# Performance work log

Measured on AMD Instinct MI355X. Metric: run time of the kernel, lower is better.

## Reference

```python
import jax, jax.numpy as jnp
import numpy as np

N_LUT_IN = 4  # fan-in of every LUT node (the 'n' init arg)
KSIZE = 3


def _lut_level(x, w):
    """x: [O, N, L*n] in [0,1]; w: [O, L, 2^n] LUT tables -> [O, N, L].
    Differentiable LUT = multilinear interpolation over the 2^n corners."""
    O, L = w.shape[0], w.shape[1]
    xi = x.reshape(x.shape[0], x.shape[1], L, N_LUT_IN)
    # iterative doubling builds corner probs without a [.., 2^n, n] broadcast
    p = jnp.ones(xi.shape[:3] + (1,), xi.dtype)
    for i in range(N_LUT_IN):
        xii = xi[..., i:i + 1]
        p = jnp.concatenate([p * (1.0 - xii), p * xii], axis=-1)  # [O,N,L,2^i+1]
    return jnp.einsum('onlc,olc->onl', p, w)


def _lut_tree(flat, ws):
    """flat: [O, N, n_leaf_inputs]; ws: list of per-level LUT tables [O, L_lvl, 16]."""
    x = jax.nn.sigmoid(flat)  # squash real activations into [0,1] for interpolation
    for li, w in enumerate(ws):
        need = w.shape[1] * N_LUT_IN
        pad = need - x.shape[-1]
        if pad > 0:  # pad with 0.5 == sigmoid(0), matching zero-padding of raw inputs
            x = jnp.pad(x, ((0, 0), (0, 0), (0, pad)), constant_values=0.5)
        x = _lut_level(x, w)
        if li < len(ws) - 1:
            x = jax.nn.sigmoid(x)
    return x[..., 0]  # [O, N]


def setup_inputs() -> dict:
    key = jax.random.key(0)
    ks = jax.random.split(key, 5)
    B, C, H, W = 8, 64, 32, 32
    O, Q = 32, 8
    x = jax.random.normal(ks[0], (B, C, H, W), jnp.float32)
    rng = np.random.default_rng(0)
    ci = jnp.asarray(np.stack([rng.permutation(C)[:Q] for _ in range(O)]), jnp.int32)
    # tree level widths for 72 leaf inputs, fan-in 4: 72 -> 18 -> 5 -> 2 -> 1
    w0 = jax.random.normal(ks[1], (O, 18, 16), jnp.float32) * 0.5
    w1 = jax.random.normal(ks[2], (O, 5, 16), jnp.float32) * 0.5
    w2 = jax.random.normal(ks[3], (O, 2, 16), jnp.float32) * 0.5
    w3 = jax.random.normal(ks[4], (O, 1, 16), jnp.float32) * 0.5
    return {'x': x, 'w0': w0, 'w1': w1, 'w2': w2, 'w3': w3, 'channel_indices': ci}


def reference(x, w0, w1, w2, w3, channel_indices):
    B, C, H, W = x.shape
    K = KSIZE
    # unfold: pad=1, stride=1 -> [B, C*K*K, Ho, Wo], feature dim is channel-major (C, K, K)
    patches = jax.lax.conv_general_dilated_patches(
        x, (K, K), (1, 1), ((1, 1), (1, 1)))
    Ho, Wo = patches.shape[2], patches.shape[3]
    patches = patches.reshape(B, C, K, K, Ho, Wo)
    O, Q = channel_indices.shape
    sel = patches[:, channel_indices]  # per-out-channel gather: [B, O, Q, K, K, Ho, Wo]
    # match torch permute(0,2,3,1,4,5): leaf order per pixel is (channel, kh, kw)
    flat = sel.transpose(1, 0, 5, 6, 2, 3, 4).reshape(O, B * Ho * Wo, Q * K * K)
    out = _lut_tree(flat, [w0, w1, w2, w3])  # [O, B*Ho*Wo]
    return out.reshape(O, B, Ho, Wo).transpose(1, 0, 2, 3)  # [B, O, Ho, Wo]
```

## Files before the change

### kernel.cpp

```cpp
#include <hip/hip_runtime.h>

#define O_DIM 32
#define Q_DIM 8
#define HW 32

__device__ __forceinline__ float sigmoidf(float v) {
    return __builtin_amdgcn_rcpf(1.0f + __expf(-v));
}

__device__ __forceinline__ float lut4(float s0, float s1, float s2, float s3,
                                      const float* __restrict__ W) {
    float a[8];
#pragma unroll
    for (int j = 0; j < 8; ++j) a[j] = fmaf(s3, W[j + 8] - W[j], W[j]);
#pragma unroll
    for (int j = 0; j < 4; ++j) a[j] = fmaf(s2, a[j + 4] - a[j], a[j]);
#pragma unroll
    for (int j = 0; j < 2; ++j) a[j] = fmaf(s1, a[j + 2] - a[j], a[j]);
    return fmaf(s0, a[1] - a[0], a[0]);
}

__global__ __launch_bounds__(256) void lt_conv_kernel(
    const float* __restrict__ x,
    const float* __restrict__ w0,
    const float* __restrict__ w1,
    const float* __restrict__ w2,
    const float* __restrict__ w3,
    const int*   __restrict__ ci,
    float*       __restrict__ out)
{
    const int bid  = blockIdx.x;
    const int tile = bid & 3;
    const int b    = (bid >> 2) & 7;
    const int o    = bid >> 5;

    const int tid = threadIdx.x;
    const int wo  = tid & 31;
    const int ho  = tile * 8 + (tid >> 5);

    float s[72];
#pragma unroll
    for (int q = 0; q < Q_DIM; ++q) {
        const int c = ci[o * Q_DIM + q];
        const float* xc = x + (size_t)(b * 64 + c) * (HW * HW);
#pragma unroll
        for (int dy = 0; dy < 3; ++dy) {
            const int y = ho + dy - 1;
            const bool yok = (unsigned)y < (unsigned)HW;
#pragma unroll
            for (int dx = 0; dx < 3; ++dx) {
                const int xx = wo + dx - 1;
                const bool ok = yok && ((unsigned)xx < (unsigned)HW);
                const float v = ok ? xc[y * HW + xx] : 0.0f;
                s[q * 9 + dy * 3 + dx] = sigmoidf(v);
            }
        }
    }

    const float* W0 = w0 + o * 18 * 16;
    float t[18];
#pragma unroll
    for (int l = 0; l < 18; ++l)
        t[l] = sigmoidf(lut4(s[4*l], s[4*l+1], s[4*l+2], s[4*l+3], W0 + l*16));

    const float* W1 = w1 + o * 5 * 16;
    float u[5];
#pragma unroll
    for (int l = 0; l < 4; ++l)
        u[l] = sigmoidf(lut4(t[4*l], t[4*l+1], t[4*l+2], t[4*l+3], W1 + l*16));
    u[4] = sigmoidf(lut4(t[16], t[17], 0.5f, 0.5f, W1 + 4*16));

    const float* W2 = w2 + o * 2 * 16;
    const float v0 = sigmoidf(lut4(u[0], u[1], u[2], u[3], W2));
    const float v1 = sigmoidf(lut4(u[4], 0.5f, 0.5f, 0.5f, W2 + 16));

    const float* W3 = w3 + o * 16;
    const float r = lut4(v0, v1, 0.5f, 0.5f, W3);

    out[((size_t)(b * O_DIM + o) * HW + ho) * HW + wo] = r;
}

extern "C" void kernel_launch(void* const* d_in, const int* in_sizes, int n_in,
                              void* d_out, int out_size, void* d_ws, size_t ws_size,
                              hipStream_t stream) {
    const float* x  = (const float*)d_in[0];
    const float* w0 = (const float*)d_in[1];
    const float* w1 = (const float*)d_in[2];
    const float* w2 = (const float*)d_in[3];
    const float* w3 = (const float*)d_in[4];
    const int*   ci = (const int*)d_in[5];
    float* out = (float*)d_out;

    dim3 grid(O_DIM * 8 * 4);
    dim3 block(256);
    lt_conv_kernel<<<grid, block, 0, stream>>>(x, w0, w1, w2, w3, ci, out);
}
```

Before: 83.68 us.

## Stage sigmoid-ed padded input tile in LDS and compute two rows per thread with packed FMA

Each block now covers a full 32x32 image for one (o,b) pair. It loads the 8 selected channels with a one-pixel halo into shared memory and applies the sigmoid once per input element, instead of once per 3x3 window tap. Each thread evaluates the LUT tree for two vertically adjacent pixels using 2-wide float vectors, which lets the compiler emit packed FMAs. The goal is to remove the 9x redundant global loads and sigmoids. The trade-offs are fewer blocks (256), about 37KB of LDS per block, and higher register pressure.

```diff
diff --git a/kernel.cpp b/kernel.cpp
--- a/kernel.cpp
+++ b/kernel.cpp
@@ -1,26 +1,34 @@
 #include <hip/hip_runtime.h>
 
-#define O_DIM 32
-#define Q_DIM 8
+typedef float v2f __attribute__((ext_vector_type(2)));
+
 #define HW 32
+#define QD 8
 
 __device__ __forceinline__ float sigmoidf(float v) {
     return __builtin_amdgcn_rcpf(1.0f + __expf(-v));
 }
 
-__device__ __forceinline__ float lut4(float s0, float s1, float s2, float s3,
-                                      const float* __restrict__ W) {
-    float a[8];
-#pragma unroll
-    for (int j = 0; j < 8; ++j) a[j] = fmaf(s3, W[j + 8] - W[j], W[j]);
-#pragma unroll
-    for (int j = 0; j < 4; ++j) a[j] = fmaf(s2, a[j + 4] - a[j], a[j]);
-#pragma unroll
-    for (int j = 0; j < 2; ++j) a[j] = fmaf(s1, a[j + 2] - a[j], a[j]);
-    return fmaf(s0, a[1] - a[0], a[0]);
+__device__ __forceinline__ v2f sig2(v2f v) {
+    v2f r; r.x = sigmoidf(v.x); r.y = sigmoidf(v.y); return r;
 }
 
-__global__ __launch_bounds__(256) void lt_conv_kernel(
+__device__ __forceinline__ v2f lut4v(const v2f* s, const float* __restrict__ W) {
+    v2f a[8];
+#pragma unroll
+    for (int j = 0; j < 8; ++j) {
+        const float d = W[j + 8] - W[j];
+        const v2f dv = {d, d}, wv = {W[j], W[j]};
+        a[j] = __builtin_elementwise_fma(s[3], dv, wv);
+    }
+#pragma unroll
+    for (int j = 0; j < 4; ++j) a[j] = __builtin_elementwise_fma(s[2], a[j + 4] - a[j], a[j]);
+#pragma unroll
+    for (int j = 0; j < 2; ++j) a[j] = __builtin_elementwise_fma(s[1], a[j + 2] - a[j], a[j]);
+    return __builtin_elementwise_fma(s[0], a[1] - a[0], a[0]);
+}
+
+__global__ __launch_bounds__(512, 4) void lt_conv_kernel(
     const float* __restrict__ x,
     const float* __restrict__ w0,
     const float* __restrict__ w1,
@@ -29,55 +37,77 @@
     const int*   __restrict__ ci,
     float*       __restrict__ out)
 {
-    const int bid  = blockIdx.x;
-    const int tile = bid & 3;
-    const int b    = (bid >> 2) & 7;
-    const int o    = bid >> 5;
+    const int o = blockIdx.x & 31;
+    const int b = blockIdx.x >> 5;
+    const int tid = threadIdx.x;
 
-    const int tid = threadIdx.x;
-    const int wo  = tid & 31;
-    const int ho  = tile * 8 + (tid >> 5);
+    __shared__ float stile[QD * 34 * 34];
+    __shared__ int   ldsci[QD];
 
-    float s[72];
+    if (tid < QD) ldsci[tid] = ci[o * QD + tid];
+    __syncthreads();
+
 #pragma unroll
-    for (int q = 0; q < Q_DIM; ++q) {
-        const int c = ci[o * Q_DIM + q];
-        const float* xc = x + (size_t)(b * 64 + c) * (HW * HW);
-#pragma unroll
-        for (int dy = 0; dy < 3; ++dy) {
-            const int y = ho + dy - 1;
-            const bool yok = (unsigned)y < (unsigned)HW;
-#pragma unroll
-            for (int dx = 0; dx < 3; ++dx) {
-                const int xx = wo + dx - 1;
-                const bool ok = yok && ((unsigned)xx < (unsigned)HW);
-                const float v = ok ? xc[y * HW + xx] : 0.0f;
-                s[q * 9 + dy * 3 + dx] = sigmoidf(v);
+    for (int it = 0; it < 19; ++it) {
+        const int idx = tid + it * 512;
+        if (idx < QD * 34 * 34) {
+            const int q   = idx / 1156;
+            const int rem = idx - q * 1156;
+            const int row = rem / 34;
+            const int col = rem - row * 34;
+            const int y = row - 1, xx = col - 1;
+            float v = 0.0f;
+            if ((unsigned)y < 32u && (unsigned)xx < 32u) {
+                const int c = ldsci[q];
+                v = x[(((size_t)b * 64 + c) * HW + y) * HW + xx];
             }
+            stile[idx] = sigmoidf(v);
         }
     }
+    __syncthreads();
+
+    const int wo = tid & 31;
+    const int r0 = (tid >> 5) * 2;
 
     const float* W0 = w0 + o * 18 * 16;
-    float t[18];
+    v2f t[18];
 #pragma unroll
-    for (int l = 0; l < 18; ++l)
-        t[l] = sigmoidf(lut4(s[4*l], s[4*l+1], s[4*l+2], s[4*l+3], W0 + l*16));
+    for (int l = 0; l < 18; ++l) {
+        v2f p[4];
+#pragma unroll
+        for (int j = 0; j < 4; ++j) {
+            const int flat = 4 * l + j;
+            const int q = flat / 9, k = flat - 9 * q;
+            const int dy = k / 3, dx = k - 3 * dy;
+            const float* base = stile + q * 1156 + (r0 + dy) * 34 + (wo + dx);
+            p[j].x = base[0];
+            p[j].y = base[34];
+        }
+        t[l] = sig2(lut4v(p, W0 + l * 16));
+    }
 
     const float* W1 = w1 + o * 5 * 16;
-    float u[5];
+    const v2f h = {0.5f, 0.5f};
+    v2f u[5];
 #pragma unroll
-    for (int l = 0; l < 4; ++l)
-        u[l] = sigmoidf(lut4(t[4*l], t[4*l+1], t[4*l+2], t[4*l+3], W1 + l*16));
-    u[4] = sigmoidf(lut4(t[16], t[17], 0.5f, 0.5f, W1 + 4*16));
+    for (int l = 0; l < 4; ++l) u[l] = sig2(lut4v(t + 4 * l, W1 + l * 16));
+    {
+        v2f p[4] = {t[16], t[17], h, h};
+        u[4] = sig2(lut4v(p, W1 + 4 * 16));
+    }
 
     const float* W2 = w2 + o * 2 * 16;
-    const float v0 = sigmoidf(lut4(u[0], u[1], u[2], u[3], W2));
-    const float v1 = sigmoidf(lut4(u[4], 0.5f, 0.5f, 0.5f, W2 + 16));
+    const v2f vv0 = sig2(lut4v(u, W2));
+    v2f p1[4] = {u[4], h, h, h};
+    const v2f vv1 = sig2(lut4v(p1, W2 + 16));
 
     const float* W3 = w3 + o * 16;
-    const float r = lut4(v0, v1, 0.5f, 0.5f, W3);
+    v2f p2[4] = {vv0, vv1, h, h};
+    const v2f res = lut4v(p2, W3);
 
-    out[((size_t)(b * O_DIM + o) * HW + ho) * HW + wo] = r;
+    float* op = out + (((size_t)b * 32 + o) * HW + r0) * HW + wo;
+    op[0]  = res.x;
+    op[HW] = res.y;
 }
 
 extern "C" void kernel_launch(void* const* d_in, const int* in_sizes, int n_in,
@@ -91,7 +121,5 @@
     const int*   ci = (const int*)d_in[5];
     float* out = (float*)d_out;
 
-    dim3 grid(O_DIM * 8 * 4);
-    dim3 block(256);
-    lt_conv_kernel<<<grid, block, 0, stream>>>(x, w0, w1, w2, w3, ci, out);
+    lt_conv_kernel<<<dim3(32 * 8), dim3(512), 0, stream>>>(x, w0, w1, w2, w3, ci, out);
 }
```

Result: faster. 80.71 us (-3.5%).
